# Optimization experiments

Measured on AMD Instinct MI355X. Metric: run time of the kernel, lower is better.

The kernel has to match this reference:

```python
import jax, jax.numpy as jnp
import numpy as np
import math

N_HEAD = 16
D_MODEL = 1024
ATT_DIM = D_MODEL // N_HEAD


def setup_inputs() -> dict:
    key = jax.random.key(0)
    ks = jax.random.split(key, 11)
    B, T, D = 2, 2048, D_MODEL
    s = 1.0 / math.sqrt(D)
    return {
        "q": jax.random.normal(ks[0], (B, T, D), jnp.float32),
        "k": jax.random.normal(ks[1], (B, T, D), jnp.float32),
        "v": jax.random.normal(ks[2], (B, T, D), jnp.float32),
        "Wq": jax.random.normal(ks[3], (D, D), jnp.float32) * s,
        "bq": jnp.zeros((D,), jnp.float32),
        "Wk": jax.random.normal(ks[4], (D, D), jnp.float32) * s,
        "bk": jnp.zeros((D,), jnp.float32),
        "Wv": jax.random.normal(ks[5], (D, D), jnp.float32) * s,
        "bv": jnp.zeros((D,), jnp.float32),
        "Wo": jax.random.normal(ks[6], (D, D), jnp.float32) * s,
        "bo": jnp.zeros((D,), jnp.float32),
    }


def reference(q, k, v, Wq, bq, Wk, bk, Wv, bv, Wo, bo):
    B, T, D = q.shape
    H, hd = N_HEAD, ATT_DIM
    # Linear projections (torch Linear: x @ W.T + b)
    qh = (q @ Wq.T + bq).reshape(B, T, H, hd).transpose(0, 2, 1, 3)  # [B,H,T,hd]
    kh = (k @ Wk.T + bk).reshape(B, T, H, hd).transpose(0, 2, 1, 3)
    vh = (v @ Wv.T + bv).reshape(B, T, H, hd).transpose(0, 2, 1, 3)
    scale = 1.0 / math.sqrt(hd)
    score = jnp.einsum("bhqd,bhkd->bhqk", qh, kh) * scale  # [B,H,T,T]
    attn = jax.nn.softmax(score, axis=-1)
    out = jnp.einsum("bhqk,bhkd->bhqd", attn, vh)  # [B,H,T,hd]
    out = out.transpose(0, 2, 1, 3).reshape(B, T, D)
    return out @ Wo.T + bo
```

## Files before the change

### kernel.cpp

```cpp
#include <hip/hip_runtime.h>


typedef __attribute__((ext_vector_type(8))) short bf16x8;
typedef __attribute__((ext_vector_type(4))) float f32x4;
typedef __attribute__((ext_vector_type(4))) unsigned int u32x4;
typedef __attribute__((ext_vector_type(2))) unsigned long long u64x2;

#define E22 ((size_t)1 << 22)
#define E20 ((size_t)1 << 20)

__device__ __forceinline__ unsigned short f2bf(float x) {
    unsigned int u = __float_as_uint(x);
    u += 0x7fffu + ((u >> 16) & 1u);
    return (unsigned short)(u >> 16);
}
__device__ __forceinline__ unsigned int pk2bf(float a, float b) {
    return __builtin_amdgcn_perm(__float_as_uint(a), __float_as_uint(b), 0x03020706u);
}
__device__ __forceinline__ void gl16(const void* g, void* l) {
    __builtin_amdgcn_global_load_lds(
        (const __attribute__((address_space(1))) void*)g,
        (__attribute__((address_space(3))) void*)l, 16, 0, 0);
}
__device__ __forceinline__ f32x4 mfma16(bf16x8 a, bf16x8 b, f32x4 c) {
    return __builtin_amdgcn_mfma_f32_16x16x32_bf16(a, b, c, 0, 0, 0);
}

__global__ __launch_bounds__(256)
void split_all(const float* __restrict__ q, const float* __restrict__ k,
               const float* __restrict__ v, const float* __restrict__ wq,
               const float* __restrict__ wk, const float* __restrict__ wv,
               const float* __restrict__ wo, unsigned short* __restrict__ ws)
{
    const size_t t = (size_t)blockIdx.x * 256 + threadIdx.x;
    const size_t e = t * 4;
    const float* src; unsigned short* dst; size_t off;
    if (e < 3 * E22) {
        const unsigned int which = (unsigned int)(e >> 22);
        src = which == 0 ? q : (which == 1 ? k : v);
        off = e & (E22 - 1);
        dst = ws + (size_t)which * E22;
    } else {
        const size_t e2 = e - 3 * E22;
        const unsigned int which = (unsigned int)(e2 >> 20);
        off = e2 & (E20 - 1);
        src = which == 0 ? wq : (which == 1 ? wk : (which == 2 ? wv : wo));
        dst = ws + 3 * E22 + (size_t)which * E20;
    }
    const float4 xv = *(const float4*)(src + off);
    ushort4 h4;
    h4.x = f2bf(xv.x); h4.y = f2bf(xv.y); h4.z = f2bf(xv.z); h4.w = f2bf(xv.w);
    *(ushort4*)(dst + off) = h4;
}

__global__ __launch_bounds__(256)
void gemm_qkv(const unsigned short* __restrict__ Xall,
              const unsigned short* __restrict__ Wcat,
              const float* __restrict__ bq, const float* __restrict__ bk,
              const float* __restrict__ bv, unsigned short* __restrict__ Qhp,
              unsigned short* __restrict__ Khp, unsigned short* __restrict__ Vtp)
{
    __shared__ unsigned short Xs[3 * 4096], Ws[3 * 4096];
    const int tid = threadIdx.x;
    const int w = tid >> 6, ln = tid & 63;
    const int quad = ln >> 4, L = ln & 15;
    const int wy = w >> 1, wx = w & 1;

    const int bid = blockIdx.x;
    const int xcd = bid & 7, j = bid >> 3;
    const int gg = xcd * 12 + (j >> 3);
    const int which = gg >> 5, m_i = gg & 31, n_i = j & 7;
    const int m0 = m_i * 128;

    const unsigned short* X = Xall + (size_t)which * E22;
    const unsigned short* W = Wcat + ((size_t)which * 1024 + n_i * 128) * 1024;
    const float* bp = which == 0 ? bq : (which == 1 ? bk : bv);
    unsigned short* outp = which == 0 ? Qhp : (which == 1 ? Khp : Vtp);
    const float qscale = which == 0 ? 0.18033688011f : 1.0f;

    const int ci0 = ln, ci1 = 64 + ln;
    const int row0 = w * 32 + (ci0 >> 2), row1 = w * 32 + (ci1 >> 2);
    const int gc0 = (ci0 & 3) ^ ((row0 >> 1) & 3);
    const int gc1 = (ci1 & 3) ^ ((row1 >> 1) & 3);
    const int lb0 = w * 2048, lb1 = w * 2048 + 1024;
    const unsigned short* Xbp = X + (size_t)m0 * 1024;
    const size_t gx0 = (size_t)row0 * 1024 + gc0 * 8;
    const size_t gx1 = (size_t)row1 * 1024 + gc1 * 8;

    f32x4 acc[4][4];
#pragma unroll
    for (int i = 0; i < 4; ++i)
#pragma unroll
        for (int jj = 0; jj < 4; ++jj) { f32x4 z = {0.f,0.f,0.f,0.f}; acc[i][jj] = z; }

#define QSTAGE(k0_, bo_)                                                       \
    do {                                                                       \
        gl16(Xbp + gx0 + (k0_), (char*)Xs + (bo_) + lb0);                      \
        gl16(W   + gx0 + (k0_), (char*)Ws + (bo_) + lb0);                      \
        gl16(Xbp + gx1 + (k0_), (char*)Xs + (bo_) + lb1);                      \
        gl16(W   + gx1 + (k0_), (char*)Ws + (bo_) + lb1);                      \
    } while (0)

#define QCOMP(eo_)                                                             \
    do {                                                                       \
        const unsigned short* Xc = Xs + (eo_);                                 \
        const unsigned short* Wc = Ws + (eo_);                                 \
        bf16x8 ah[4], bh[4];                                                   \
        _Pragma("unroll")                                                      \
        for (int mt = 0; mt < 4; ++mt) {                                       \
            const int row = wy * 64 + mt * 16 + L;                             \
            ah[mt] = *(const bf16x8*)(Xc + row * 32 +                          \
                                      ((quad ^ ((row >> 1) & 3)) * 8));        \
        }                                                                      \
        _Pragma("unroll")                                                      \
        for (int nt = 0; nt < 4; ++nt) {                                       \
            const int row = wx * 64 + nt * 16 + L;                             \
            bh[nt] = *(const bf16x8*)(Wc + row * 32 +                          \
                                      ((quad ^ ((row >> 1) & 3)) * 8));        \
        }                                                                      \
        _Pragma("unroll")                                                      \
        for (int mt = 0; mt < 4; ++mt)                                         \
            _Pragma("unroll")                                                  \
            for (int nt = 0; nt < 4; ++nt)                                     \
                acc[mt][nt] = mfma16(ah[mt], bh[nt], acc[mt][nt]);             \
    } while (0)

    QSTAGE(0, 0);
    QSTAGE(32, 8192);

    int cur = 0;
    for (int kt = 0; kt < 31; ++kt) {
        asm volatile("s_waitcnt vmcnt(4)" ::: "memory");
        __builtin_amdgcn_s_barrier();
        asm volatile("" ::: "memory");
        if (kt < 30) {
            int st = cur + 2; if (st >= 3) st -= 3;
            QSTAGE((kt + 2) * 32, st * 8192);
        }
        QCOMP(cur * 4096);
        cur = (cur == 2) ? 0 : cur + 1;
    }
    asm volatile("s_waitcnt vmcnt(0)" ::: "memory");
    __builtin_amdgcn_s_barrier();
    asm volatile("" ::: "memory");
    QCOMP(cur * 4096);
#undef QSTAGE
#undef QCOMP

#pragma unroll
    for (int mt = 0; mt < 4; ++mt)
#pragma unroll
        for (int nt = 0; nt < 4; ++nt) {
            const int gm0 = m0 + wy * 64 + mt * 16 + quad * 4;
            const int bn  = n_i * 128 + wx * 64 + nt * 16 + L;
            const float bvv = bp[bn];
            const int hh = bn >> 6, dd = bn & 63;
            if (which < 2) {
#pragma unroll
                for (int r = 0; r < 4; ++r) {
                    const int gm = gm0 + r;
                    const int bb = gm >> 11, tt = gm & 2047;
                    outp[((size_t)(bb * 16 + hh) * 2048 + tt) * 64 + dd] =
                        f2bf((acc[mt][nt][r] + bvv) * qscale);
                }
            } else {
                const int bb = gm0 >> 11, t0 = gm0 & 2047;
                ushort4 pk;
                pk.x = f2bf(acc[mt][nt][0] + bvv);
                pk.y = f2bf(acc[mt][nt][1] + bvv);
                pk.z = f2bf(acc[mt][nt][2] + bvv);
                pk.w = f2bf(acc[mt][nt][3] + bvv);
                *(ushort4*)(outp + ((size_t)(bb * 16 + hh) * 64 + dd) * 2048 + t0) = pk;
            }
        }
}

__global__ __launch_bounds__(256)
void gemm_out(const unsigned short* __restrict__ X, const unsigned short* __restrict__ W,
              const float* __restrict__ bias, float* __restrict__ outp)
{
    __shared__ unsigned short Xs[3 * 4096], Ws[3 * 2048];
    const int tid = threadIdx.x;
    const int w = tid >> 6, ln = tid & 63;
    const int quad = ln >> 4, L = ln & 15;

    const int bid = blockIdx.x;
    const int xcd = bid & 7, j = bid >> 3;
    const int m0 = (xcd * 4 + (j >> 4)) * 128;
    const int n0 = (j & 15) * 64;

    const int cix0 = ln, cix1 = 64 + ln;
    const int rowx0 = w * 32 + (cix0 >> 2), rowx1 = w * 32 + (cix1 >> 2);
    const int gcx0 = (cix0 & 3) ^ ((rowx0 >> 1) & 3);
    const int gcx1 = (cix1 & 3) ^ ((rowx1 >> 1) & 3);
    const int roww = w * 16 + (ln >> 2);
    const int gcw = (ln & 3) ^ ((roww >> 1) & 3);
    const size_t gxx0 = (size_t)(m0 + rowx0) * 1024 + gcx0 * 8;
    const size_t gxx1 = (size_t)(m0 + rowx1) * 1024 + gcx1 * 8;
    const size_t gww  = (size_t)(n0 + roww) * 1024 + gcw * 8;

    f32x4 acc[2][4];
#pragma unroll
    for (int i = 0; i < 2; ++i)
#pragma unroll
        for (int jj = 0; jj < 4; ++jj) { f32x4 z = {0.f,0.f,0.f,0.f}; acc[i][jj] = z; }

#define OSTAGE(k0_, bf_)                                                       \
    do {                                                                       \
        gl16(X + gxx0 + (k0_), (char*)Xs + (bf_) * 8192 + w * 2048);           \
        gl16(X + gxx1 + (k0_), (char*)Xs + (bf_) * 8192 + w * 2048 + 1024);    \
        gl16(W + gww  + (k0_), (char*)Ws + (bf_) * 4096 + w * 1024);           \
    } while (0)

#define OCOMP(bf_)                                                             \
    do {                                                                       \
        const unsigned short* Xc = Xs + (bf_) * 4096;                          \
        const unsigned short* Wc = Ws + (bf_) * 2048;                          \
        bf16x8 ah[2], bh[4];                                                   \
        _Pragma("unroll")                                                      \
        for (int mt = 0; mt < 2; ++mt) {                                       \
            const int row = w * 32 + mt * 16 + L;                              \
            ah[mt] = *(const bf16x8*)(Xc + row * 32 +                          \
                                      ((quad ^ ((row >> 1) & 3)) * 8));        \
        }                                                                      \
        _Pragma("unroll")                                                      \
        for (int nt = 0; nt < 4; ++nt) {                                       \
            const int row = nt * 16 + L;                                       \
            bh[nt] = *(const bf16x8*)(Wc + row * 32 +                          \
                                      ((quad ^ ((row >> 1) & 3)) * 8));        \
        }                                                                      \
        _Pragma("unroll")                                                      \
        for (int mt = 0; mt < 2; ++mt)                                         \
            _Pragma("unroll")                                                  \
            for (int nt = 0; nt < 4; ++nt)                                     \
                acc[mt][nt] = mfma16(ah[mt], bh[nt], acc[mt][nt]);             \
    } while (0)

    OSTAGE(0, 0);
    OSTAGE(32, 1);

    int cur = 0;
    for (int kt = 0; kt < 31; ++kt) {
        asm volatile("s_waitcnt vmcnt(3)" ::: "memory");
        __builtin_amdgcn_s_barrier();
        asm volatile("" ::: "memory");
        if (kt < 30) {
            int st = cur + 2; if (st >= 3) st -= 3;
            OSTAGE((kt + 2) * 32, st);
        }
        OCOMP(cur);
        cur = (cur == 2) ? 0 : cur + 1;
    }
    asm volatile("s_waitcnt vmcnt(0)" ::: "memory");
    __builtin_amdgcn_s_barrier();
    asm volatile("" ::: "memory");
    OCOMP(cur);
#undef OSTAGE
#undef OCOMP

#pragma unroll
    for (int mt = 0; mt < 2; ++mt)
#pragma unroll
        for (int nt = 0; nt < 4; ++nt) {
            const int gm0 = m0 + w * 32 + mt * 16 + quad * 4;
            const int gn  = n0 + nt * 16 + L;
            const float bvv = bias[gn];
#pragma unroll
            for (int r = 0; r < 4; ++r)
                outp[(size_t)(gm0 + r) * 1024 + gn] = acc[mt][nt][r] + bvv;
        }
}

__global__ __launch_bounds__(256, 2)
void flash(const unsigned short* __restrict__ Qh, const unsigned short* __restrict__ Kh,
           const unsigned short* __restrict__ Vt, unsigned short* __restrict__ A)
{
    __shared__ unsigned short SM[24576];
    __shared__ float Lsc[2 * 4 * 64];
    const int tid = threadIdx.x;
    const int w = tid >> 6, ln = tid & 63;
    const int quad = ln >> 4, L = ln & 15;
    const int wq = w & 1, wk = w >> 1;

    const int bid = blockIdx.x;
    const int xcd = bid & 7, j = bid >> 3;
    const int bh_i = xcd * 4 + (j & 3);
    const int qt = j >> 2;
    const int b = bh_i >> 4, h = bh_i & 15;

    const unsigned short* Qb = Qh + ((size_t)bh_i * 2048 + qt * 128 + wq * 64) * 64;
    const unsigned short* Kb = Kh + ((size_t)bh_i * 2048 + wk * 32) * 64;
    const unsigned short* Vb = Vt + (size_t)bh_i * 64 * 2048 + wk * 32;

    bf16x8 bq[4][2];
#pragma unroll
    for (int nt = 0; nt < 4; ++nt)
#pragma unroll
        for (int kc = 0; kc < 2; ++kc)
            bq[nt][kc] = *(const bf16x8*)(Qb + (nt * 16 + L) * 64 + kc * 32 + quad * 8);

    const short one_bf = (short)0x3F80;
    bf16x8 bone = {one_bf, one_bf, one_bf, one_bf, one_bf, one_bf, one_bf, one_bf};

    f32x4 o[4][4];
    f32x4 lacc[4];
#pragma unroll
    for (int mtd = 0; mtd < 4; ++mtd)
#pragma unroll
        for (int nt = 0; nt < 4; ++nt) { f32x4 z = {0.f,0.f,0.f,0.f}; o[mtd][nt] = z; }
#pragma unroll
    for (int nt = 0; nt < 4; ++nt) { f32x4 z = {0.f,0.f,0.f,0.f}; lacc[nt] = z; }

    const int rl  = ln >> 3;
    const int gck = (ln & 7) ^ rl;
    char* Kw = (char*)SM + w * 12288;

#define KSTAGE(kt_, bo_)                                                        \
    do {                                                                        \
        _Pragma("unroll")                                                       \
        for (int i_ = 0; i_ < 4; ++i_)                                          \
            gl16(Kb + (size_t)((kt_) * 64 + i_ * 8 + rl) * 64 + gck * 8,        \
                 Kw + (bo_) + i_ * 1024);                                       \
    } while (0)

#define VLOAD(kt_, dst_)                                                        \
    do {                                                                        \
        _Pragma("unroll")                                                       \
        for (int m_ = 0; m_ < 4; ++m_) {                                        \
            const unsigned short* Vr = Vb + (size_t)(m_ * 16 + L) * 2048 +      \
                                       (kt_) * 64 + quad * 4;                   \
            u64x2 t_;                                                           \
            t_.x = *(const unsigned long long*)(Vr);                            \
            t_.y = *(const unsigned long long*)(Vr + 16);                       \
            dst_[m_] = __builtin_bit_cast(bf16x8, t_);                          \
        }                                                                       \
    } while (0)

#define COMP(bo_, av_)                                                          \
    do {                                                                        \
        const char* Kc = Kw + (bo_);                                            \
        bf16x8 ak[2][2];                                                        \
        _Pragma("unroll")                                                       \
        for (int mt = 0; mt < 2; ++mt)                                          \
            _Pragma("unroll")                                                   \
            for (int kc = 0; kc < 2; ++kc)                                      \
                ak[mt][kc] = *(const bf16x8*)(Kc + (mt * 16 + L) * 128 +        \
                                              (((kc * 4 + quad) ^ (L & 7)) * 16)); \
        f32x4 s[2][4];                                                          \
        _Pragma("unroll")                                                       \
        for (int mt = 0; mt < 2; ++mt)                                          \
            _Pragma("unroll")                                                   \
            for (int nt = 0; nt < 4; ++nt) {                                    \
                f32x4 z = {0.f, 0.f, 0.f, 0.f};                                 \
                z = mfma16(ak[mt][0], bq[nt][0], z);                            \
                z = mfma16(ak[mt][1], bq[nt][1], z);                            \
                s[mt][nt] = z;                                                  \
            }                                                                   \
        bf16x8 pbx[4];                                                          \
        _Pragma("unroll")                                                       \
        for (int nt = 0; nt < 4; ++nt) {                                        \
            u32x4 pd;                                                           \
            pd.x = pk2bf(__builtin_amdgcn_exp2f(s[0][nt][0]),                   \
                         __builtin_amdgcn_exp2f(s[0][nt][1]));                  \
            pd.y = pk2bf(__builtin_amdgcn_exp2f(s[0][nt][2]),                   \
                         __builtin_amdgcn_exp2f(s[0][nt][3]));                  \
            pd.z = pk2bf(__builtin_amdgcn_exp2f(s[1][nt][0]),                   \
                         __builtin_amdgcn_exp2f(s[1][nt][1]));                  \
            pd.w = pk2bf(__builtin_amdgcn_exp2f(s[1][nt][2]),                   \
                         __builtin_amdgcn_exp2f(s[1][nt][3]));                  \
            pbx[nt] = __builtin_bit_cast(bf16x8, pd);                           \
        }                                                                       \
        _Pragma("unroll")                                                       \
        for (int mtd = 0; mtd < 4; ++mtd)                                       \
            _Pragma("unroll")                                                   \
            for (int nt = 0; nt < 4; ++nt)                                      \
                o[mtd][nt] = mfma16(av_[mtd], pbx[nt], o[mtd][nt]);             \
        _Pragma("unroll")                                                       \
        for (int nt = 0; nt < 4; ++nt)                                          \
            lacc[nt] = mfma16(bone, pbx[nt], lacc[nt]);                         \
    } while (0)

    bf16x8 avA[4], avB[4];
    VLOAD(0, avA); KSTAGE(0, 0);
    VLOAD(1, avB); KSTAGE(1, 4096);

    int bo = 0, bs = 8192;
#pragma unroll 1
    for (int kt = 0; kt < 30; kt += 2) {
        asm volatile("s_waitcnt vmcnt(12)" ::: "memory");
        COMP(bo, avA);
        VLOAD(kt + 2, avA);
        KSTAGE(kt + 2, bs);
        bo = (bo == 8192) ? 0 : bo + 4096;
        bs = (bs == 8192) ? 0 : bs + 4096;
        asm volatile("s_waitcnt vmcnt(12)" ::: "memory");
        COMP(bo, avB);
        VLOAD(kt + 3, avB);
        KSTAGE(kt + 3, bs);
        bo = (bo == 8192) ? 0 : bo + 4096;
        bs = (bs == 8192) ? 0 : bs + 4096;
    }
    asm volatile("s_waitcnt vmcnt(12)" ::: "memory");
    COMP(bo, avA);
    bo = (bo == 8192) ? 0 : bo + 4096;
    asm volatile("s_waitcnt vmcnt(0)" ::: "memory");
    COMP(bo, avB);
#undef KSTAGE
#undef VLOAD
#undef COMP

    __syncthreads();
    float* Rb = (float*)SM;
    if (wk == 1) {
#pragma unroll
        for (int mtd = 0; mtd < 4; ++mtd)
#pragma unroll
            for (int nt = 0; nt < 4; ++nt)
                *(f32x4*)(Rb + wq * 4096 + (mtd * 4 + nt) * 256 + ln * 4) = o[mtd][nt];
#pragma unroll
        for (int nt = 0; nt < 4; ++nt)
            Lsc[wq * 256 + nt * 64 + ln] = lacc[nt][0];
    }
    __syncthreads();
    if (wk == 0) {
#pragma unroll
        for (int mtd = 0; mtd < 4; ++mtd)
#pragma unroll
            for (int nt = 0; nt < 4; ++nt)
                o[mtd][nt] += *(const f32x4*)(Rb + wq * 4096 + (mtd * 4 + nt) * 256 + ln * 4);

#pragma unroll
        for (int nt = 0; nt < 4; ++nt) {
            const float lsum = lacc[nt][0] + Lsc[wq * 256 + nt * 64 + ln];
            const float inv = 1.0f / lsum;
            const int qrow = b * 2048 + qt * 128 + wq * 64 + nt * 16 + L;
#pragma unroll
            for (int mtd = 0; mtd < 4; ++mtd) {
                const int d0 = mtd * 16 + quad * 4;
                ushort4 pk;
                pk.x = f2bf(o[mtd][nt][0] * inv);
                pk.y = f2bf(o[mtd][nt][1] * inv);
                pk.z = f2bf(o[mtd][nt][2] * inv);
                pk.w = f2bf(o[mtd][nt][3] * inv);
                *(ushort4*)(A + (size_t)qrow * 1024 + h * 64 + d0) = pk;
            }
        }
    }
}

extern "C" void kernel_launch(void* const* d_in, const int* in_sizes, int n_in,
                              void* d_out, int out_size, void* d_ws, size_t ws_size,
                              hipStream_t stream) {
    const float* q  = (const float*)d_in[0];
    const float* k  = (const float*)d_in[1];
    const float* v  = (const float*)d_in[2];
    const float* Wq = (const float*)d_in[3];
    const float* bq = (const float*)d_in[4];
    const float* Wk = (const float*)d_in[5];
    const float* bk = (const float*)d_in[6];
    const float* Wv = (const float*)d_in[7];
    const float* bv = (const float*)d_in[8];
    const float* Wo = (const float*)d_in[9];
    const float* bo = (const float*)d_in[10];

    unsigned short* W = (unsigned short*)d_ws;
    unsigned short *Xall = W;
    unsigned short *Wcat = W + 3 * E22;
    unsigned short *Wob  = Wcat + 3 * E20;
    unsigned short *Qhp  = W + 4 * E22;
    unsigned short *Khp  = W + 5 * E22;
    unsigned short *Vtp  = W + 6 * E22;
    unsigned short *A    = W;

    split_all<<<16384, 256, 0, stream>>>(q, k, v, Wq, Wk, Wv, Wo, W);

    gemm_qkv<<<768, 256, 0, stream>>>(Xall, Wcat, bq, bk, bv, Qhp, Khp, Vtp);

    flash<<<512, 256, 0, stream>>>(Qhp, Khp, Vtp, A);

    gemm_out<<<512, 256, 0, stream>>>(A, Wob, bo, (float*)d_out);
}
```

Baseline: 244.6 us.

## Load K and V tiles directly into registers with permuted V layout

The V-projection epilogue now writes V-transposed with a permuted token order inside each 32-token group, so the flash kernel can fetch each V fragment with one 16-byte load instead of two 8-byte loads. K tiles are no longer staged through LDS with global_load_lds; each lane loads its K fragments straight from global memory into registers, and the manual vmcnt waits and LDS ring buffer are removed. This cuts LDS traffic and LDS footprint, which may raise occupancy. In exchange the K loads become strided per-lane global reads, and the compiler now schedules the waits.

```diff
diff --git a/kernel.cpp b/kernel.cpp
--- a/kernel.cpp
+++ b/kernel.cpp
@@ -4,7 +4,6 @@
 typedef __attribute__((ext_vector_type(8))) short bf16x8;
 typedef __attribute__((ext_vector_type(4))) float f32x4;
 typedef __attribute__((ext_vector_type(4))) unsigned int u32x4;
-typedef __attribute__((ext_vector_type(2))) unsigned long long u64x2;
 
 #define E22 ((size_t)1 << 22)
 #define E20 ((size_t)1 << 20)
@@ -165,12 +164,14 @@
                 }
             } else {
                 const int bb = gm0 >> 11, t0 = gm0 & 2047;
+                const int c5 = t0 & 31;
+                const int p0 = (t0 & ~31) | (((c5 & 15) >> 2) << 3) | ((c5 >> 4) << 2);
                 ushort4 pk;
                 pk.x = f2bf(acc[mt][nt][0] + bvv);
                 pk.y = f2bf(acc[mt][nt][1] + bvv);
                 pk.z = f2bf(acc[mt][nt][2] + bvv);
                 pk.w = f2bf(acc[mt][nt][3] + bvv);
-                *(ushort4*)(outp + ((size_t)(bb * 16 + hh) * 64 + dd) * 2048 + t0) = pk;
+                *(ushort4*)(outp + ((size_t)(bb * 16 + hh) * 64 + dd) * 2048 + p0) = pk;
             }
         }
 }
@@ -275,7 +276,7 @@
 void flash(const unsigned short* __restrict__ Qh, const unsigned short* __restrict__ Kh,
            const unsigned short* __restrict__ Vt, unsigned short* __restrict__ A)
 {
-    __shared__ unsigned short SM[24576];
+    __shared__ float Rb[8192];
     __shared__ float Lsc[2 * 4 * 64];
     const int tid = threadIdx.x;
     const int w = tid >> 6, ln = tid & 63;
@@ -289,8 +290,8 @@
     const int b = bh_i >> 4, h = bh_i & 15;
 
     const unsigned short* Qb = Qh + ((size_t)bh_i * 2048 + qt * 128 + wq * 64) * 64;
-    const unsigned short* Kb = Kh + ((size_t)bh_i * 2048 + wk * 32) * 64;
-    const unsigned short* Vb = Vt + (size_t)bh_i * 64 * 2048 + wk * 32;
+    const unsigned short* Kp = Kh + ((size_t)bh_i * 2048 + wk * 32 + L) * 64 + quad * 8;
+    const unsigned short* Vp = Vt + (size_t)bh_i * 64 * 2048 + (size_t)L * 2048 + wk * 32 + quad * 8;
 
     bf16x8 bq[4][2];
 #pragma unroll
@@ -311,49 +312,34 @@
 #pragma unroll
     for (int nt = 0; nt < 4; ++nt) { f32x4 z = {0.f,0.f,0.f,0.f}; lacc[nt] = z; }
 
-    const int rl  = ln >> 3;
-    const int gck = (ln & 7) ^ rl;
-    char* Kw = (char*)SM + w * 12288;
-
-#define KSTAGE(kt_, bo_)                                                        \
+#define KLOAD(kt_, dst_)                                                        \
     do {                                                                        \
         _Pragma("unroll")                                                       \
-        for (int i_ = 0; i_ < 4; ++i_)                                          \
-            gl16(Kb + (size_t)((kt_) * 64 + i_ * 8 + rl) * 64 + gck * 8,        \
-                 Kw + (bo_) + i_ * 1024);                                       \
+        for (int mt_ = 0; mt_ < 2; ++mt_)                                       \
+            _Pragma("unroll")                                                   \
+            for (int kc_ = 0; kc_ < 2; ++kc_)                                   \
+                dst_[mt_][kc_] = *(const bf16x8*)(Kp +                          \
+                    (size_t)((kt_) * 64 + mt_ * 16) * 64 + kc_ * 32);           \
     } while (0)
 
 #define VLOAD(kt_, dst_)                                                        \
     do {                                                                        \
         _Pragma("unroll")                                                       \
-        for (int m_ = 0; m_ < 4; ++m_) {                                        \
-            const unsigned short* Vr = Vb + (size_t)(m_ * 16 + L) * 2048 +      \
-                                       (kt_) * 64 + quad * 4;                   \
-            u64x2 t_;                                                           \
-            t_.x = *(const unsigned long long*)(Vr);                            \
-            t_.y = *(const unsigned long long*)(Vr + 16);                       \
-            dst_[m_] = __builtin_bit_cast(bf16x8, t_);                          \
-        }                                                                       \
-    } while (0)
-
-#define COMP(bo_, av_)                                                          \
+        for (int m_ = 0; m_ < 4; ++m_)                                          \
+            dst_[m_] = *(const bf16x8*)(Vp + (size_t)(m_ * 16) * 2048 +         \
+                                        (kt_) * 64);                            \
+    } while (0)
+
+#define COMP(k_, v_)                                                            \
     do {                                                                        \
-        const char* Kc = Kw + (bo_);                                            \
-        bf16x8 ak[2][2];                                                        \
-        _Pragma("unroll")                                                       \
-        for (int mt = 0; mt < 2; ++mt)                                          \
-            _Pragma("unroll")                                                   \
-            for (int kc = 0; kc < 2; ++kc)                                      \
-                ak[mt][kc] = *(const bf16x8*)(Kc + (mt * 16 + L) * 128 +        \
-                                              (((kc * 4 + quad) ^ (L & 7)) * 16)); \
         f32x4 s[2][4];                                                          \
         _Pragma("unroll")                                                       \
         for (int mt = 0; mt < 2; ++mt)                                          \
             _Pragma("unroll")                                                   \
             for (int nt = 0; nt < 4; ++nt) {                                    \
                 f32x4 z = {0.f, 0.f, 0.f, 0.f};                                 \
-                z = mfma16(ak[mt][0], bq[nt][0], z);                            \
-                z = mfma16(ak[mt][1], bq[nt][1], z);                            \
+                z = mfma16(k_[mt][0], bq[nt][0], z);                            \
+                z = mfma16(k_[mt][1], bq[nt][1], z);                            \
                 s[mt][nt] = z;                                                  \
             }                                                                   \
         bf16x8 pbx[4];                                                          \
@@ -374,43 +360,30 @@
         for (int mtd = 0; mtd < 4; ++mtd)                                       \
             _Pragma("unroll")                                                   \
             for (int nt = 0; nt < 4; ++nt)                                      \
-                o[mtd][nt] = mfma16(av_[mtd], pbx[nt], o[mtd][nt]);             \
+                o[mtd][nt] = mfma16(v_[mtd], pbx[nt], o[mtd][nt]);              \
         _Pragma("unroll")                                                       \
         for (int nt = 0; nt < 4; ++nt)                                          \
             lacc[nt] = mfma16(bone, pbx[nt], lacc[nt]);                         \
     } while (0)
 
-    bf16x8 avA[4], avB[4];
-    VLOAD(0, avA); KSTAGE(0, 0);
-    VLOAD(1, avB); KSTAGE(1, 4096);
-
-    int bo = 0, bs = 8192;
+    bf16x8 kA[2][2], kB[2][2], vA[4], vB[4];
+    KLOAD(0, kA); VLOAD(0, vA);
+    KLOAD(1, kB); VLOAD(1, vB);
+
 #pragma unroll 1
     for (int kt = 0; kt < 30; kt += 2) {
-        asm volatile("s_waitcnt vmcnt(12)" ::: "memory");
-        COMP(bo, avA);
-        VLOAD(kt + 2, avA);
-        KSTAGE(kt + 2, bs);
-        bo = (bo == 8192) ? 0 : bo + 4096;
-        bs = (bs == 8192) ? 0 : bs + 4096;
-        asm volatile("s_waitcnt vmcnt(12)" ::: "memory");
-        COMP(bo, avB);
-        VLOAD(kt + 3, avB);
-        KSTAGE(kt + 3, bs);
-        bo = (bo == 8192) ? 0 : bo + 4096;
-        bs = (bs == 8192) ? 0 : bs + 4096;
-    }
-    asm volatile("s_waitcnt vmcnt(12)" ::: "memory");
-    COMP(bo, avA);
-    bo = (bo == 8192) ? 0 : bo + 4096;
-    asm volatile("s_waitcnt vmcnt(0)" ::: "memory");
-    COMP(bo, avB);
-#undef KSTAGE
+        COMP(kA, vA);
+        KLOAD(kt + 2, kA); VLOAD(kt + 2, vA);
+        COMP(kB, vB);
+        KLOAD(kt + 3, kB); VLOAD(kt + 3, vB);
+    }
+    COMP(kA, vA);
+    COMP(kB, vB);
+#undef KLOAD
 #undef VLOAD
 #undef COMP
 
     __syncthreads();
-    float* Rb = (float*)SM;
     if (wk == 1) {
 #pragma unroll
         for (int mtd = 0; mtd < 4; ++mtd)
```

Result: faster. 237.3 us (-3.0%).
